# Kernel optimization log

Measured on AMD Instinct MI355X. Metric: run time of the kernel, lower is better.

Reference implementation:

```python
import jax, jax.numpy as jnp
import numpy as np

N, M = 50000, 20
EVEN, ODD, EDGE = 64, 64, 32
CAT = 2 * EVEN + EDGE + ODD  # even_i | even_j | nbr_fea | odd_cross


def _w(k, fan_in, fan_out):
    return jax.random.normal(k, (fan_in, fan_out), jnp.float32) * (1.0 / np.sqrt(fan_in))


def setup_inputs() -> dict:
    key = jax.random.key(0)
    ks = jax.random.split(key, 16)
    return dict(
        even_node=jax.random.normal(ks[0], (N, EVEN), jnp.float32),
        odd_node=jax.random.normal(ks[1], (N, ODD), jnp.float32),
        nbr_fea=jax.random.normal(ks[2], (N, M, EDGE), jnp.float32),
        nbr_fea_idx=jax.random.randint(ks[3], (N, M), 0, N),
        W_em1=_w(ks[4], CAT, EVEN), b_em1=jnp.zeros((EVEN,), jnp.float32),
        W_eg=_w(ks[5], EVEN, EVEN), b_eg=jnp.zeros((EVEN,), jnp.float32),
        W_em2=_w(ks[6], EVEN, EVEN), b_em2=jnp.zeros((EVEN,), jnp.float32),
        W_pej=_w(ks[7], EVEN, ODD), b_pej=jnp.zeros((ODD,), jnp.float32),
        W_pei=_w(ks[8], EVEN, ODD), b_pei=jnp.zeros((ODD,), jnp.float32),
        W_om1=_w(ks[9], 2 * ODD, ODD),  # no bias
        W_ogh=_w(ks[10], CAT, ODD), b_ogh=jnp.zeros((ODD,), jnp.float32),
        W_og=_w(ks[11], ODD, ODD), b_og=jnp.zeros((ODD,), jnp.float32),
    )


def reference(even_node, odd_node, nbr_fea, nbr_fea_idx,
              W_em1, b_em1, W_eg, b_eg, W_em2, b_em2,
              W_pej, b_pej, W_pei, b_pei, W_om1,
              W_ogh, b_ogh, W_og, b_og):
    # Gather neighbor features: [N, M, F]
    even_j = jnp.take(even_node, nbr_fea_idx, axis=0)
    odd_j = jnp.take(odd_node, nbr_fea_idx, axis=0)
    even_i = jnp.broadcast_to(even_node[:, None, :], even_j.shape)
    odd_i = odd_node[:, None, :]
    odd_cross = odd_i * odd_j  # [N, M, ODD]

    # shared concat input [N, M, CAT]
    cat_in = jnp.concatenate(
        [even_i, even_j, nbr_fea, jnp.broadcast_to(odd_cross, (even_j.shape[0], even_j.shape[1], odd_cross.shape[-1]))],
        axis=-1)

    # even channel: Dense -> softplus -> gate * msg -> sum over neighbors
    even_h = jax.nn.softplus(cat_in @ W_em1 + b_em1)
    even_gate = jax.nn.sigmoid(even_h @ W_eg + b_eg)
    even_msg = jax.nn.softplus(even_h @ W_em2 + b_em2)
    even_agg = jnp.sum(even_gate * even_msg, axis=1)  # [N, EVEN]

    # odd channel: equivariant products, tanh value, gated sum
    odd_ie = odd_i * (even_j @ W_pej + b_pej)
    odd_ei = (even_i @ W_pei + b_pei) * odd_j
    odd_value = jnp.tanh(jnp.concatenate([odd_ie, odd_ei], axis=-1) @ W_om1)
    odd_gate = jax.nn.sigmoid(jax.nn.softplus(cat_in @ W_ogh + b_ogh) @ W_og + b_og)
    odd_agg = jnp.sum(odd_gate * odd_value, axis=1)  # [N, ODD]

    return (even_node + even_agg, odd_node + odd_agg)
```

## Files before the change

### kernel.cpp

```cpp
#include <hip/hip_runtime.h>


#define NN    50000
#define GN    4
#define MT    5
#define CSTR  168
#define ESTR  72
#define IOSTR 136
#define RSTR  68

#define LDS_A   0
#define LDS_EH  26880
#define LDS_OH  38400
#define LDS_OI  49920
#define LDS_EI  50944
#define LDS_PG  51456
#define LDS_SZ  52992

typedef __attribute__((ext_vector_type(8))) short  short8;
typedef __attribute__((ext_vector_type(4))) float  floatx4;

__device__ unsigned char g_wbuf[114688];

#define OFF_EM1 0
#define OFF_OGH 28672
#define OFF_EG  57344
#define OFF_EM2 65536
#define OFF_OG  73728
#define OFF_PEJ 81920
#define OFF_PEI 90112
#define OFF_OM1 98304

__device__ __forceinline__ unsigned short f2b(float x) {
    unsigned u = __float_as_uint(x);
    return (unsigned short)((u + 0x7fffu + ((u >> 16) & 1u)) >> 16);
}
__device__ __forceinline__ float b2f(unsigned short s) {
    return __uint_as_float(((unsigned)s) << 16);
}
__device__ __forceinline__ float spf(float x) {
    return fmaxf(x, 0.f) + __logf(1.f + __expf(-fabsf(x)));
}
__device__ __forceinline__ float sgf(float x) {
    return __builtin_amdgcn_rcpf(1.f + __expf(-x));
}
__device__ __forceinline__ float thf(float x) {
    float e = __expf(-2.f * fabsf(x));
    float t = (1.f - e) * __builtin_amdgcn_rcpf(1.f + e);
    return __builtin_copysignf(t, x);
}
__device__ __forceinline__ floatx4 mfma16(short8 a, short8 b, floatx4 c) {
    return __builtin_amdgcn_mfma_f32_16x16x32_bf16(a, b, c, 0, 0, 0);
}
__device__ __forceinline__ short8 wfrag(int base, int s, int t, int l) {
    return *(const short8*)(g_wbuf + base + ((size_t)((s * 4 + t) * 64 + l)) * 16);
}

__global__ __launch_bounds__(256) void prepack(
    const float* __restrict__ W_em1, const float* __restrict__ W_ogh,
    const float* __restrict__ W_eg,  const float* __restrict__ W_em2,
    const float* __restrict__ W_og,  const float* __restrict__ W_pej,
    const float* __restrict__ W_pei, const float* __restrict__ W_om1)
{
    int tid = blockIdx.x * 256 + threadIdx.x;
    int gid = tid >> 6, l = tid & 63;
    const float* W; int base, gl;
    if      (gid < 28) { W = W_em1; base = OFF_EM1; gl = gid;      }
    else if (gid < 56) { W = W_ogh; base = OFF_OGH; gl = gid - 28; }
    else if (gid < 64) { W = W_eg;  base = OFF_EG;  gl = gid - 56; }
    else if (gid < 72) { W = W_em2; base = OFF_EM2; gl = gid - 64; }
    else if (gid < 80) { W = W_og;  base = OFF_OG;  gl = gid - 72; }
    else if (gid < 88) { W = W_pej; base = OFF_PEJ; gl = gid - 80; }
    else if (gid < 96) { W = W_pei; base = OFF_PEI; gl = gid - 88; }
    else               { W = W_om1; base = OFF_OM1; gl = gid - 96; }
    int s = gl >> 2, t = gl & 3;
    int k0 = s * 32 + (l >> 4) * 8;
    int n  = t * 16 + (l & 15);
    short8 pk;
    #pragma unroll
    for (int j = 0; j < 8; ++j) pk[j] = (short)f2b(W[(size_t)(k0 + j) * 64 + n]);
    *(short8*)(g_wbuf + base + ((size_t)((s * 4 + t) * 64 + l)) * 16) = pk;
}

__global__ __launch_bounds__(256, 3) void eoconv_mfma(
    const float* __restrict__ even_node, const float* __restrict__ odd_node,
    const float* __restrict__ nbr_fea,   const int* __restrict__ nbr_idx,
    const float* __restrict__ b_em1, const float* __restrict__ b_eg,
    const float* __restrict__ b_em2, const float* __restrict__ b_pej,
    const float* __restrict__ b_pei, const float* __restrict__ b_ogh,
    const float* __restrict__ b_og,  float* __restrict__ out)
{
    extern __shared__ char smem[];
    short* sh_cat = (short*)(smem + LDS_A);
    short* sh_io  = (short*)(smem + LDS_A);
    float* red_e  = (float*)(smem + LDS_A);
    short* sh_eh  = (short*)(smem + LDS_EH);
    float* red_o  = (float*)(smem + LDS_EH);
    short* sh_oh  = (short*)(smem + LDS_OH);
    float* sh_oi  = (float*)(smem + LDS_OI);
    short* sh_ei  = (short*)(smem + LDS_EI);
    short* sh_pg  = (short*)(smem + LDS_PG);

    const int w  = threadIdx.x >> 6;
    const int l  = threadIdx.x & 63;
    const int n0 = blockIdx.x * GN;

    const float eif = even_node[(long)(n0 + w) * 64 + l];
    const float oif = odd_node [(long)(n0 + w) * 64 + l];
    sh_oi[w * 64 + l] = oif;
    sh_ei[w * 64 + l] = (short)f2b(eif);
    #pragma unroll 2
    for (int i2 = 0; i2 < 20; i2 += 2) {
        const int  ii = i2 + (l >> 5);
        const int  cc = l & 31;
        const long p  = (long)(n0 + w) * 20 + ii;
        sh_cat[(w * 20 + ii) * CSTR + 64 + cc] = (short)f2b(nbr_fea[p * 32 + cc]);
    }
    #pragma unroll 4
    for (int i = 0; i < 20; ++i) {
        const int  r = w * 20 + i;
        const long p = (long)(n0 + w) * 20 + i;
        const int  j = nbr_idx[p];
        const float ejf = even_node[(long)j * 64 + l];
        const float ojf = odd_node [(long)j * 64 + l];
        sh_cat[r * CSTR + l]      = (short)f2b(ejf);
        sh_cat[r * CSTR + 96 + l] = (short)f2b(oif * ojf);
        sh_oh [r * ESTR + l]      = (short)f2b(ojf);
    }
    __syncthreads();

    const int col = w * 16 + (l & 15);
    const int q8  = (l >> 4) * 8;
    const int q4  = (l >> 4) * 4;
    const float be1 = b_em1[col], bgh = b_ogh[col], bpi = b_pei[col], bpj = b_pej[col];
    const floatx4 z4 = {0.f, 0.f, 0.f, 0.f};

    {
        floatx4 Tm = z4, Tg = z4, Tp = z4;
        #pragma unroll
        for (int ks = 0; ks < 2; ++ks) {
            short8 Ae = *(const short8*)&sh_ei[((l & 3)) * 64 + ks * 32 + q8];
            Tm = mfma16(Ae, wfrag(OFF_EM1, ks, w, l), Tm);
            Tg = mfma16(Ae, wfrag(OFF_OGH, ks, w, l), Tg);
            Tp = mfma16(Ae, wfrag(OFF_PEI, ks, w, l), Tp);
        }
        if (l < 16) {
            #pragma unroll
            for (int rg = 0; rg < 4; ++rg) {
                sh_pg[      rg * 64 + col] = (short)f2b(Tm[rg] + be1);
                sh_pg[256 + rg * 64 + col] = (short)f2b(Tg[rg] + bgh);
                sh_pg[512 + rg * 64 + col] = (short)f2b(Tp[rg] + bpi);
            }
        }
    }

    floatx4 C1[MT], Cg[MT], Cpj[MT];
    #pragma unroll
    for (int t = 0; t < MT; ++t) { C1[t] = z4; Cg[t] = z4; Cpj[t] = z4; }
    #pragma unroll
    for (int ks = 0; ks < 5; ++ks) {
        short8 B1 = wfrag(OFF_EM1, ks + 2, w, l);
        short8 Bg = wfrag(OFF_OGH, ks + 2, w, l);
        short8 Bx = B1;
        if (ks < 2) Bx = wfrag(OFF_PEJ, ks, w, l);
        const int ko = ks * 32 + q8;
        #pragma unroll
        for (int t = 0; t < MT; ++t) {
            short8 A = *(const short8*)&sh_cat[(t * 16 + (l & 15)) * CSTR + ko];
            C1[t] = mfma16(A, B1, C1[t]);
            Cg[t] = mfma16(A, Bg, Cg[t]);
            if (ks < 2) Cpj[t] = mfma16(A, Bx, Cpj[t]);
        }
    }

    unsigned pk[MT][4];
    #pragma unroll
    for (int t = 0; t < MT; ++t) {
        const int r0 = t * 16 + q4;
        const int g  = r0 / 20;
        const float em1g = b2f((unsigned short)sh_pg[      g * 64 + col]);
        const float oghg = b2f((unsigned short)sh_pg[256 + g * 64 + col]);
        const float peig = b2f((unsigned short)sh_pg[512 + g * 64 + col]);
        const float oi   = sh_oi[g * 64 + col];
        float ojv[4];
        #pragma unroll
        for (int rg = 0; rg < 4; ++rg)
            ojv[rg] = b2f((unsigned short)sh_oh[(r0 + rg) * ESTR + col]);
        #pragma unroll
        for (int rg = 0; rg < 4; ++rg) {
            const int row = r0 + rg;
            const float pj = Cpj[t][rg] + bpj;
            pk[t][rg] = (unsigned)f2b(oi * pj) | ((unsigned)f2b(peig * ojv[rg]) << 16);
            sh_eh[row * ESTR + col] = (short)f2b(spf(C1[t][rg] + em1g));
            sh_oh[row * ESTR + col] = (short)f2b(spf(Cg[t][rg] + oghg));
        }
    }
    __syncthreads();

    #pragma unroll
    for (int t = 0; t < MT; ++t) {
        #pragma unroll
        for (int rg = 0; rg < 4; ++rg) {
            const int row = t * 16 + q4 + rg;
            sh_io[row * IOSTR + col]      = (short)(pk[t][rg] & 0xffffu);
            sh_io[row * IOSTR + 64 + col] = (short)(pk[t][rg] >> 16);
        }
    }

    floatx4 Gg[MT], Gm[MT], Go[MT];
    #pragma unroll
    for (int t = 0; t < MT; ++t) { Gg[t] = z4; Gm[t] = z4; Go[t] = z4; }
    #pragma unroll
    for (int ks = 0; ks < 2; ++ks) {
        short8 Beg = wfrag(OFF_EG,  ks, w, l);
        short8 Bm2 = wfrag(OFF_EM2, ks, w, l);
        short8 Bog = wfrag(OFF_OG,  ks, w, l);
        const int ko = ks * 32 + q8;
        #pragma unroll
        for (int t = 0; t < MT; ++t) {
            short8 Ae = *(const short8*)&sh_eh[(t * 16 + (l & 15)) * ESTR + ko];
            short8 Ao = *(const short8*)&sh_oh[(t * 16 + (l & 15)) * ESTR + ko];
            Gg[t] = mfma16(Ae, Beg, Gg[t]);
            Gm[t] = mfma16(Ae, Bm2, Gm[t]);
            Go[t] = mfma16(Ao, Bog, Go[t]);
        }
    }
    __syncthreads();

    floatx4 Gt[MT];
    #pragma unroll
    for (int t = 0; t < MT; ++t) Gt[t] = z4;
    #pragma unroll
    for (int ks = 0; ks < 4; ++ks) {
        short8 Bo = wfrag(OFF_OM1, ks, w, l);
        const int ko = ks * 32 + q8;
        #pragma unroll
        for (int t = 0; t < MT; ++t) {
            short8 Ai = *(const short8*)&sh_io[(t * 16 + (l & 15)) * IOSTR + ko];
            Gt[t] = mfma16(Ai, Bo, Gt[t]);
        }
    }
    __syncthreads();

    {
        const float beg = b_eg[col], bm2 = b_em2[col], bog = b_og[col];
        #pragma unroll
        for (int t = 0; t < MT; ++t) {
            #pragma unroll
            for (int rg = 0; rg < 4; ++rg) {
                const int row = t * 16 + q4 + rg;
                red_e[row * RSTR + col] = sgf(Gg[t][rg] + beg) * spf(Gm[t][rg] + bm2);
                red_o[row * RSTR + col] = sgf(Go[t][rg] + bog) * thf(Gt[t][rg]);
            }
        }
    }
    __syncthreads();

    {
        float se = 0.f, so = 0.f;
        #pragma unroll 4
        for (int i = 0; i < 20; ++i) {
            se += red_e[(w * 20 + i) * RSTR + l];
            so += red_o[(w * 20 + i) * RSTR + l];
        }
        const long nb = (long)(n0 + w) * 64 + l;
        out[nb]                 = eif + se;
        out[(long)NN * 64 + nb] = oif + so;
    }
}

extern "C" void kernel_launch(void* const* d_in, const int* in_sizes, int n_in,
                              void* d_out, int out_size, void* d_ws, size_t ws_size,
                              hipStream_t stream) {
    const float* even_node = (const float*)d_in[0];
    const float* odd_node  = (const float*)d_in[1];
    const float* nbr_fea   = (const float*)d_in[2];
    const int*   nbr_idx   = (const int*)d_in[3];
    const float* W_em1 = (const float*)d_in[4];
    const float* b_em1 = (const float*)d_in[5];
    const float* W_eg  = (const float*)d_in[6];
    const float* b_eg  = (const float*)d_in[7];
    const float* W_em2 = (const float*)d_in[8];
    const float* b_em2 = (const float*)d_in[9];
    const float* W_pej = (const float*)d_in[10];
    const float* b_pej = (const float*)d_in[11];
    const float* W_pei = (const float*)d_in[12];
    const float* b_pei = (const float*)d_in[13];
    const float* W_om1 = (const float*)d_in[14];
    const float* W_ogh = (const float*)d_in[15];
    const float* b_ogh = (const float*)d_in[16];
    const float* W_og  = (const float*)d_in[17];
    const float* b_og  = (const float*)d_in[18];

    static int s_attr_done = 0;
    if (!s_attr_done) {
        (void)hipFuncSetAttribute((const void*)eoconv_mfma,
                                  hipFuncAttributeMaxDynamicSharedMemorySize, LDS_SZ);
        s_attr_done = 1;
    }

    prepack<<<dim3(28), dim3(256), 0, stream>>>(W_em1, W_ogh, W_eg, W_em2,
                                                W_og, W_pej, W_pei, W_om1);
    eoconv_mfma<<<dim3(NN / GN), dim3(256), LDS_SZ, stream>>>(
        even_node, odd_node, nbr_fea, nbr_idx,
        b_em1, b_eg, b_em2, b_pej, b_pei, b_ogh, b_og,
        (float*)d_out);
}
```

Before: 535.8 us.

## Interleave neighbor rows across nodes, swizzle LDS, and reduce aggregation in registers

Rows of the tile are renumbered as neighbour*4+node, so every 16-row MFMA tile holds one fixed node per row group. The per-node precomputed terms can then be read once per lane, and the neighbour sum is done in registers with cross-lane shuffles instead of an LDS reduction buffer. The LDS layout drops padded strides in favour of XOR swizzling, shrinks the footprint and raises launch bounds to 4 blocks per CU. Gathers use float4 loads and packed bf16 conversion via v_cvt_pk_bf16_f32, at the cost of extra barriers and more intricate indexing.

```diff
diff --git a/kernel.cpp b/kernel.cpp
--- a/kernel.cpp
+++ b/kernel.cpp
@@ -4,18 +4,18 @@
 #define NN    50000
 #define GN    4
 #define MT    5
-#define CSTR  168
-#define ESTR  72
-#define IOSTR 136
-#define RSTR  68
-
-#define LDS_A   0
-#define LDS_EH  26880
-#define LDS_OH  38400
-#define LDS_OI  49920
-#define LDS_EI  50944
-#define LDS_PG  51456
-#define LDS_SZ  52992
+#define ECSTR 128
+#define NSTR  40
+#define ESTR  64
+#define IOSTR 128
+
+#define LDS_EJC 0
+#define LDS_NBR 20480
+#define LDS_OJ  26880
+#define LDS_OIB 37120
+#define LDS_EIB 37632
+#define LDS_PG  38144
+#define LDS_SZ  39680
 
 typedef __attribute__((ext_vector_type(8))) short  short8;
 typedef __attribute__((ext_vector_type(4))) float  floatx4;
@@ -31,6 +31,11 @@
 #define OFF_PEI 90112
 #define OFF_OM1 98304
 
+__device__ __forceinline__ unsigned cvtpk(float lo, float hi) {
+    unsigned r;
+    asm("v_cvt_pk_bf16_f32 %0, %1, %2" : "=v"(r) : "v"(lo), "v"(hi));
+    return r;
+}
 __device__ __forceinline__ unsigned short f2b(float x) {
     unsigned u = __float_as_uint(x);
     return (unsigned short)((u + 0x7fffu + ((u >> 16) & 1u)) >> 16);
@@ -82,7 +87,7 @@
     *(short8*)(g_wbuf + base + ((size_t)((s * 4 + t) * 64 + l)) * 16) = pk;
 }
 
-__global__ __launch_bounds__(256, 3) void eoconv_mfma(
+__global__ __launch_bounds__(256, 4) void eoconv_mfma(
     const float* __restrict__ even_node, const float* __restrict__ odd_node,
     const float* __restrict__ nbr_fea,   const int* __restrict__ nbr_idx,
     const float* __restrict__ b_em1, const float* __restrict__ b_eg,
@@ -91,14 +96,14 @@
     const float* __restrict__ b_og,  float* __restrict__ out)
 {
     extern __shared__ char smem[];
-    short* sh_cat = (short*)(smem + LDS_A);
-    short* sh_io  = (short*)(smem + LDS_A);
-    float* red_e  = (float*)(smem + LDS_A);
-    short* sh_eh  = (short*)(smem + LDS_EH);
-    float* red_o  = (float*)(smem + LDS_EH);
-    short* sh_oh  = (short*)(smem + LDS_OH);
-    float* sh_oi  = (float*)(smem + LDS_OI);
-    short* sh_ei  = (short*)(smem + LDS_EI);
+    short* sh_ejc = (short*)(smem + LDS_EJC);
+    short* sh_eh  = (short*)(smem + LDS_EJC);
+    short* sh_oh  = (short*)(smem + LDS_EJC + 10240);
+    short* sh_io  = (short*)(smem + LDS_EJC);
+    short* sh_nbr = (short*)(smem + LDS_NBR);
+    short* sh_oj  = (short*)(smem + LDS_OJ);
+    short* sh_oib = (short*)(smem + LDS_OIB);
+    short* sh_eib = (short*)(smem + LDS_EIB);
     short* sh_pg  = (short*)(smem + LDS_PG);
 
     const int w  = threadIdx.x >> 6;
@@ -107,31 +112,42 @@
 
     const float eif = even_node[(long)(n0 + w) * 64 + l];
     const float oif = odd_node [(long)(n0 + w) * 64 + l];
-    sh_oi[w * 64 + l] = oif;
-    sh_ei[w * 64 + l] = (short)f2b(eif);
-    #pragma unroll 2
-    for (int i2 = 0; i2 < 20; i2 += 2) {
-        const int  ii = i2 + (l >> 5);
-        const int  cc = l & 31;
-        const long p  = (long)(n0 + w) * 20 + ii;
-        sh_cat[(w * 20 + ii) * CSTR + 64 + cc] = (short)f2b(nbr_fea[p * 32 + cc]);
-    }
-    #pragma unroll 4
-    for (int i = 0; i < 20; ++i) {
-        const int  r = w * 20 + i;
-        const long p = (long)(n0 + w) * 20 + i;
-        const int  j = nbr_idx[p];
-        const float ejf = even_node[(long)j * 64 + l];
-        const float ojf = odd_node [(long)j * 64 + l];
-        sh_cat[r * CSTR + l]      = (short)f2b(ejf);
-        sh_cat[r * CSTR + 96 + l] = (short)f2b(oif * ojf);
-        sh_oh [r * ESTR + l]      = (short)f2b(ojf);
+    sh_oib[w * 64 + l] = (short)cvtpk(oif, oif);
+    sh_eib[w * 64 + l] = (short)cvtpk(eif, eif);
+
+    const long jb = (long)(n0 + w) * 20;
+    int jv[5];
+    #pragma unroll
+    for (int c = 0; c < 5; ++c) jv[c] = nbr_idx[jb + c * 4 + (l >> 4)];
+
+    const int c0 = (l & 15) * 4;
+    float oi0 = __shfl(oif, c0), oi1 = __shfl(oif, c0 + 1);
+    float oi2 = __shfl(oif, c0 + 2), oi3 = __shfl(oif, c0 + 3);
+
+    #pragma unroll
+    for (int c = 0; c < 5; ++c) {
+        const int  iw  = c * 4 + (l >> 4);
+        const int  row = iw * 4 + w;
+        const int  j   = jv[c];
+        const int  sz  = (row & 7) << 3;
+        const float4 ej4 = *(const float4*)&even_node[(long)j * 64 + c0];
+        const float4 oj4 = *(const float4*)&odd_node [(long)j * 64 + c0];
+        *(int2*)&sh_ejc[(row * ECSTR + c0) ^ sz] =
+            make_int2((int)cvtpk(ej4.x, ej4.y), (int)cvtpk(ej4.z, ej4.w));
+        *(int2*)&sh_ejc[(row * ECSTR + 64 + c0) ^ sz] =
+            make_int2((int)cvtpk(oi0 * oj4.x, oi1 * oj4.y),
+                      (int)cvtpk(oi2 * oj4.z, oi3 * oj4.w));
+        *(int2*)&sh_oj[(row * ESTR + c0) ^ sz] =
+            make_int2((int)cvtpk(oj4.x, oj4.y), (int)cvtpk(oj4.z, oj4.w));
+        const float2 nb2 = *(const float2*)&nbr_fea[(jb + iw) * 32 + (l & 15) * 2];
+        *(int*)&sh_nbr[row * NSTR + (l & 15) * 2] = (int)cvtpk(nb2.x, nb2.y);
     }
     __syncthreads();
 
     const int col = w * 16 + (l & 15);
     const int q8  = (l >> 4) * 8;
     const int q4  = (l >> 4) * 4;
+    const int lsz = (l & 7) << 3;
     const float be1 = b_em1[col], bgh = b_ogh[col], bpi = b_pei[col], bpj = b_pej[col];
     const floatx4 z4 = {0.f, 0.f, 0.f, 0.f};
 
@@ -139,7 +155,7 @@
         floatx4 Tm = z4, Tg = z4, Tp = z4;
         #pragma unroll
         for (int ks = 0; ks < 2; ++ks) {
-            short8 Ae = *(const short8*)&sh_ei[((l & 3)) * 64 + ks * 32 + q8];
+            short8 Ae = *(const short8*)&sh_eib[(l & 3) * 64 + ks * 32 + q8];
             Tm = mfma16(Ae, wfrag(OFF_EM1, ks, w, l), Tm);
             Tg = mfma16(Ae, wfrag(OFF_OGH, ks, w, l), Tg);
             Tp = mfma16(Ae, wfrag(OFF_PEI, ks, w, l), Tp);
@@ -147,9 +163,9 @@
         if (l < 16) {
             #pragma unroll
             for (int rg = 0; rg < 4; ++rg) {
-                sh_pg[      rg * 64 + col] = (short)f2b(Tm[rg] + be1);
-                sh_pg[256 + rg * 64 + col] = (short)f2b(Tg[rg] + bgh);
-                sh_pg[512 + rg * 64 + col] = (short)f2b(Tp[rg] + bpi);
+                sh_pg[      rg * 64 + col] = (short)cvtpk(Tm[rg] + be1, 0.f);
+                sh_pg[256 + rg * 64 + col] = (short)cvtpk(Tg[rg] + bgh, 0.f);
+                sh_pg[512 + rg * 64 + col] = (short)cvtpk(Tp[rg] + bpi, 0.f);
             }
         }
     }
@@ -166,46 +182,45 @@
         const int ko = ks * 32 + q8;
         #pragma unroll
         for (int t = 0; t < MT; ++t) {
-            short8 A = *(const short8*)&sh_cat[(t * 16 + (l & 15)) * CSTR + ko];
+            const int row = t * 16 + (l & 15);
+            short8 A;
+            if (ks == 2) A = *(const short8*)&sh_nbr[row * NSTR + q8];
+            else         A = *(const short8*)&sh_ejc[(row * ECSTR +
+                                (ks < 2 ? ko : ko - 32)) ^ lsz];
             C1[t] = mfma16(A, B1, C1[t]);
             Cg[t] = mfma16(A, Bg, Cg[t]);
             if (ks < 2) Cpj[t] = mfma16(A, Bx, Cpj[t]);
         }
     }
+    __syncthreads();
 
     unsigned pk[MT][4];
-    #pragma unroll
-    for (int t = 0; t < MT; ++t) {
-        const int r0 = t * 16 + q4;
-        const int g  = r0 / 20;
-        const float em1g = b2f((unsigned short)sh_pg[      g * 64 + col]);
-        const float oghg = b2f((unsigned short)sh_pg[256 + g * 64 + col]);
-        const float peig = b2f((unsigned short)sh_pg[512 + g * 64 + col]);
-        const float oi   = sh_oi[g * 64 + col];
-        float ojv[4];
-        #pragma unroll
-        for (int rg = 0; rg < 4; ++rg)
-            ojv[rg] = b2f((unsigned short)sh_oh[(r0 + rg) * ESTR + col]);
+    {
+        float em1g[4], oghg[4], peig[4], oiv[4];
         #pragma unroll
         for (int rg = 0; rg < 4; ++rg) {
-            const int row = r0 + rg;
-            const float pj = Cpj[t][rg] + bpj;
-            pk[t][rg] = (unsigned)f2b(oi * pj) | ((unsigned)f2b(peig * ojv[rg]) << 16);
-            sh_eh[row * ESTR + col] = (short)f2b(spf(C1[t][rg] + em1g));
-            sh_oh[row * ESTR + col] = (short)f2b(spf(Cg[t][rg] + oghg));
-        }
-    }
-    __syncthreads();
-
-    #pragma unroll
-    for (int t = 0; t < MT; ++t) {
-        #pragma unroll
-        for (int rg = 0; rg < 4; ++rg) {
-            const int row = t * 16 + q4 + rg;
-            sh_io[row * IOSTR + col]      = (short)(pk[t][rg] & 0xffffu);
-            sh_io[row * IOSTR + 64 + col] = (short)(pk[t][rg] >> 16);
-        }
-    }
+            em1g[rg] = b2f((unsigned short)sh_pg[      rg * 64 + col]);
+            oghg[rg] = b2f((unsigned short)sh_pg[256 + rg * 64 + col]);
+            peig[rg] = b2f((unsigned short)sh_pg[512 + rg * 64 + col]);
+            oiv [rg] = b2f((unsigned short)sh_oib[rg * 64 + col]);
+        }
+        #pragma unroll
+        for (int t = 0; t < MT; ++t) {
+            #pragma unroll
+            for (int rg = 0; rg < 4; ++rg) {
+                const int row = t * 16 + q4 + rg;
+                const int sz  = (row & 7) << 3;
+                const float ojr = b2f((unsigned short)sh_oj[(row * ESTR + col) ^ sz]);
+                const float pj  = Cpj[t][rg] + bpj;
+                pk[t][rg] = cvtpk(oiv[rg] * pj, peig[rg] * ojr);
+                const float ehv = spf(C1[t][rg] + em1g[rg]);
+                const float ohv = spf(Cg[t][rg] + oghg[rg]);
+                sh_eh[(row * ESTR + col) ^ sz] = (short)cvtpk(ehv, 0.f);
+                sh_oh[(row * ESTR + col) ^ sz] = (short)cvtpk(ohv, 0.f);
+            }
+        }
+    }
+    __syncthreads();
 
     floatx4 Gg[MT], Gm[MT], Go[MT];
     #pragma unroll
@@ -218,13 +233,36 @@
         const int ko = ks * 32 + q8;
         #pragma unroll
         for (int t = 0; t < MT; ++t) {
-            short8 Ae = *(const short8*)&sh_eh[(t * 16 + (l & 15)) * ESTR + ko];
-            short8 Ao = *(const short8*)&sh_oh[(t * 16 + (l & 15)) * ESTR + ko];
+            const int row = t * 16 + (l & 15);
+            short8 Ae = *(const short8*)&sh_eh[(row * ESTR + ko) ^ lsz];
+            short8 Ao = *(const short8*)&sh_oh[(row * ESTR + ko) ^ lsz];
             Gg[t] = mfma16(Ae, Beg, Gg[t]);
             Gm[t] = mfma16(Ae, Bm2, Gm[t]);
             Go[t] = mfma16(Ao, Bog, Go[t]);
         }
     }
+
+    float acc_e[4] = {0.f, 0.f, 0.f, 0.f};
+    {
+        const float beg = b_eg[col], bm2 = b_em2[col];
+        #pragma unroll
+        for (int t = 0; t < MT; ++t)
+            #pragma unroll
+            for (int rg = 0; rg < 4; ++rg)
+                acc_e[rg] += sgf(Gg[t][rg] + beg) * spf(Gm[t][rg] + bm2);
+    }
+    __syncthreads();
+
+    #pragma unroll
+    for (int t = 0; t < MT; ++t) {
+        #pragma unroll
+        for (int rg = 0; rg < 4; ++rg) {
+            const int row = t * 16 + q4 + rg;
+            const int sz  = (row & 7) << 3;
+            sh_io[(row * IOSTR + col) ^ sz]      = (short)pk[t][rg];
+            sh_io[(row * IOSTR + 64 + col) ^ sz] = (short)(pk[t][rg] >> 16);
+        }
+    }
     __syncthreads();
 
     floatx4 Gt[MT];
@@ -236,36 +274,37 @@
         const int ko = ks * 32 + q8;
         #pragma unroll
         for (int t = 0; t < MT; ++t) {
-            short8 Ai = *(const short8*)&sh_io[(t * 16 + (l & 15)) * IOSTR + ko];
+            const int row = t * 16 + (l & 15);
+            short8 Ai = *(const short8*)&sh_io[(row * IOSTR + ko) ^ lsz];
             Gt[t] = mfma16(Ai, Bo, Gt[t]);
         }
     }
-    __syncthreads();
-
-    {
-        const float beg = b_eg[col], bm2 = b_em2[col], bog = b_og[col];
-        #pragma unroll
-        for (int t = 0; t < MT; ++t) {
+
+    float acc_o[4] = {0.f, 0.f, 0.f, 0.f};
+    {
+        const float bog = b_og[col];
+        #pragma unroll
+        for (int t = 0; t < MT; ++t)
             #pragma unroll
-            for (int rg = 0; rg < 4; ++rg) {
-                const int row = t * 16 + q4 + rg;
-                red_e[row * RSTR + col] = sgf(Gg[t][rg] + beg) * spf(Gm[t][rg] + bm2);
-                red_o[row * RSTR + col] = sgf(Go[t][rg] + bog) * thf(Gt[t][rg]);
-            }
-        }
-    }
-    __syncthreads();
-
-    {
-        float se = 0.f, so = 0.f;
-        #pragma unroll 4
-        for (int i = 0; i < 20; ++i) {
-            se += red_e[(w * 20 + i) * RSTR + l];
-            so += red_o[(w * 20 + i) * RSTR + l];
-        }
-        const long nb = (long)(n0 + w) * 64 + l;
-        out[nb]                 = eif + se;
-        out[(long)NN * 64 + nb] = oif + so;
+            for (int rg = 0; rg < 4; ++rg)
+                acc_o[rg] += sgf(Go[t][rg] + bog) * thf(Gt[t][rg]);
+    }
+    #pragma unroll
+    for (int rg = 0; rg < 4; ++rg) {
+        acc_e[rg] += __shfl_xor(acc_e[rg], 16);
+        acc_e[rg] += __shfl_xor(acc_e[rg], 32);
+        acc_o[rg] += __shfl_xor(acc_o[rg], 16);
+        acc_o[rg] += __shfl_xor(acc_o[rg], 32);
+    }
+    {
+        const int q = l >> 4;
+        const float se = q == 0 ? acc_e[0] : q == 1 ? acc_e[1]
+                       : q == 2 ? acc_e[2] : acc_e[3];
+        const float so = q == 0 ? acc_o[0] : q == 1 ? acc_o[1]
+                       : q == 2 ? acc_o[2] : acc_o[3];
+        const long nb = (long)(n0 + q) * 64 + col;
+        out[nb]                 = even_node[nb] + se;
+        out[(long)NN * 64 + nb] = odd_node [nb] + so;
     }
 }
 
```

Result: faster. 516.5 us (-3.6%).
